# Kernel optimization log

Measured on AMD Instinct MI355X. Metric: run time of the kernel, lower is better.

Reference implementation:

```python
import jax, jax.numpy as jnp
import numpy as np

N_NODES = 50000
N_EDGES = 500000
N_FEAT = 128
EMB_DIM = 1024
HIDDEN = 128
OUT_DIM = 10
VOCAB = 55049
N_GRAPHS = 64


def setup_inputs() -> dict:
    key = jax.random.key(0)
    ks = jax.random.split(key, 12)
    x = jax.random.normal(ks[0], (N_NODES, N_FEAT), dtype=jnp.float32)
    edge_weight = jax.random.uniform(ks[1], (N_EDGES,), dtype=jnp.float32)
    edge_index = jax.random.randint(ks[2], (2, N_EDGES), 0, N_NODES)
    batch = jnp.sort(jax.random.randint(ks[3], (N_NODES,), 0, N_GRAPHS))
    node_ids = jax.random.randint(ks[4], (N_NODES,), 0, VOCAB)
    emb_table = jax.random.normal(ks[5], (VOCAB, EMB_DIM), dtype=jnp.float32)
    d_in = N_FEAT + EMB_DIM
    W1 = jax.random.normal(ks[6], (d_in, HIDDEN), dtype=jnp.float32) / np.sqrt(d_in)
    b1 = jnp.zeros((HIDDEN,), dtype=jnp.float32)
    W2 = jax.random.normal(ks[7], (HIDDEN, HIDDEN), dtype=jnp.float32) / np.sqrt(HIDDEN)
    b2 = jnp.zeros((HIDDEN,), dtype=jnp.float32)
    fcW = jax.random.normal(ks[8], (HIDDEN, OUT_DIM), dtype=jnp.float32) / np.sqrt(HIDDEN)
    fcb = jnp.zeros((OUT_DIM,), dtype=jnp.float32)
    return dict(x=x, edge_weight=edge_weight, emb_table=emb_table, W1=W1, b1=b1,
                W2=W2, b2=b2, fcW=fcW, fcb=fcb,
                edge_index=edge_index, batch=batch, node_ids=node_ids)


def gcn_conv(x, edge_index, edge_weight, W, b, n_nodes):
    # PyG GCNConv: x' = D^{-1/2} (A + I) D^{-1/2} (x W) + b, self-loop weight = 1
    x = x @ W
    src, dst = edge_index[0], edge_index[1]
    loop = jnp.arange(n_nodes)
    src = jnp.concatenate([src, loop])
    dst = jnp.concatenate([dst, loop])
    ew = jnp.concatenate([edge_weight, jnp.ones((n_nodes,), x.dtype)])
    deg = jax.ops.segment_sum(ew, dst, num_segments=n_nodes)
    dinv = jnp.where(deg > 0, jax.lax.rsqrt(deg), 0.0)
    norm = dinv[src] * ew * dinv[dst]  # [E+N]
    msgs = norm[:, None] * x[src]      # [E+N, H] gather
    out = jax.ops.segment_sum(msgs, dst, num_segments=n_nodes)  # scatter-add
    return out + b


def reference(x, edge_weight, emb_table, W1, b1, W2, b2, fcW, fcb,
              edge_index, batch, node_ids):
    n = x.shape[0]
    h = jnp.concatenate([x, emb_table[node_ids]], axis=1)  # [N, F+E]
    h = jax.nn.relu(gcn_conv(h, edge_index, edge_weight, W1, b1, n))
    h = jax.nn.relu(gcn_conv(h, edge_index, edge_weight, W2, b2, n))
    # global mean pool per graph (dropout is identity in eval)
    sums = jax.ops.segment_sum(h, batch, num_segments=N_GRAPHS)
    counts = jax.ops.segment_sum(jnp.ones((n,), h.dtype), batch, num_segments=N_GRAPHS)
    pooled = sums / jnp.maximum(counts, 1.0)[:, None]
    return pooled @ fcW + fcb
```

## Files before the change

kernel.cpp:

```cpp
#include <hip/hip_runtime.h>
#include <hip/hip_bf16.h>

#define N_NODES 50000
#define N_EDGES 500000
#define N_FEAT 128
#define EMB_DIM 1024
#define HIDDEN 128
#define OUT_DIM 10
#define N_GRAPHS 64
#define NB_NODE 196

typedef __attribute__((ext_vector_type(8))) short short8;
typedef __attribute__((ext_vector_type(4))) float f32x4;

__device__ __forceinline__ unsigned short f2bf(float f) {
    unsigned int u = __float_as_uint(f);
    return (unsigned short)((u + 0x7fffu + ((u >> 16) & 1u)) >> 16);
}
__device__ __forceinline__ float bflo(unsigned int r) { return __uint_as_float(r << 16); }
__device__ __forceinline__ float bfhi(unsigned int r) { return __uint_as_float(r & 0xffff0000u); }

__global__ __launch_bounds__(256) void k_init(float* __restrict__ deg,
                                              int* __restrict__ cnt,
                                              float* __restrict__ sums,
                                              float* __restrict__ counts) {
    int i = blockIdx.x * 256 + threadIdx.x;
    if (i < N_NODES) { deg[i] = 1.0f; cnt[i] = 0; }
    if (i < N_GRAPHS * HIDDEN) sums[i] = 0.0f;
    if (i < N_GRAPHS) counts[i] = 0.0f;
}

__global__ __launch_bounds__(256) void k_deg(const int* __restrict__ dst,
                                             const float* __restrict__ ew,
                                             float* __restrict__ deg,
                                             int* __restrict__ cnt) {
    int e = blockIdx.x * 256 + threadIdx.x;
    if (e < N_EDGES) {
        int d = dst[e];
        atomicAdd(&deg[d], ew[e]);
        atomicAdd(&cnt[d], 1);
    }
}

__global__ __launch_bounds__(256) void k_scan1(const int* __restrict__ cnt,
                                               int* __restrict__ bsum) {
    __shared__ int wsum[4];
    int i = blockIdx.x * 256 + threadIdx.x;
    int v = (i < N_NODES) ? cnt[i] : 0;
#pragma unroll
    for (int off = 32; off; off >>= 1) v += __shfl_down(v, off, 64);
    if ((threadIdx.x & 63) == 0) wsum[threadIdx.x >> 6] = v;
    __syncthreads();
    if (threadIdx.x == 0) bsum[blockIdx.x] = wsum[0] + wsum[1] + wsum[2] + wsum[3];
}

__global__ __launch_bounds__(256) void k_scan2(int* __restrict__ bsum) {
    __shared__ int sh[256];
    int t = threadIdx.x;
    int v = (t < NB_NODE) ? bsum[t] : 0;
    sh[t] = v;
    __syncthreads();
    for (int off = 1; off < 256; off <<= 1) {
        int add = (t >= off) ? sh[t - off] : 0;
        __syncthreads();
        sh[t] += add;
        __syncthreads();
    }
    if (t < NB_NODE) bsum[t] = sh[t] - v;
}

__global__ __launch_bounds__(256) void k_scan3(int* __restrict__ cntcur,
                                               const int* __restrict__ bofs,
                                               int* __restrict__ rowptr,
                                               float* __restrict__ dinv) {
    __shared__ int sh[256];
    const int t = threadIdx.x;
    const int i = blockIdx.x * 256 + t;
    int v = (i < N_NODES) ? cntcur[i] : 0;
    sh[t] = v;
    __syncthreads();
    for (int off = 1; off < 256; off <<= 1) {
        int add = (t >= off) ? sh[t - off] : 0;
        __syncthreads();
        sh[t] += add;
        __syncthreads();
    }
    int ex = sh[t] - v + bofs[blockIdx.x];
    if (i < N_NODES) {
        rowptr[i] = ex;
        cntcur[i] = ex;
        dinv[i] = 1.0f / sqrtf(dinv[i]);
    }
    if (i == 0) rowptr[N_NODES] = N_EDGES;
}

__global__ __launch_bounds__(256) void k_fill(const int* __restrict__ src,
                                              const int* __restrict__ dst,
                                              const float* __restrict__ ew,
                                              const float* __restrict__ dinv,
                                              int* __restrict__ cursor,
                                              int2* __restrict__ csr) {
    int e = blockIdx.x * 256 + threadIdx.x;
    if (e >= N_EDGES) return;
    int s = src[e], d = dst[e];
    int pos = atomicAdd(&cursor[d], 1);
    float norm = dinv[s] * ew[e] * dinv[d];
    csr[pos] = make_int2(s, __float_as_int(norm));
}

__device__ __forceinline__ void prep_one(const float* __restrict__ W,
                                         unsigned short* __restrict__ Wt,
                                         int K, int t) {
    int n = t & 127;
    int c = t >> 7;
    if (c * 16 >= K) return;
    short8 h0, h1;
#pragma unroll
    for (int i = 0; i < 16; i++) {
        unsigned short h = f2bf(W[(size_t)(c * 16 + i) * HIDDEN + n]);
        if (i < 8) h0[i] = (short)h;
        else       h1[i - 8] = (short)h;
    }
    size_t o = (size_t)n * K + c * 16;
    *(short8*)&Wt[o] = h0;
    *(short8*)&Wt[o + 8] = h1;
}

__global__ __launch_bounds__(256) void k_prep(const float* __restrict__ W1,
                                              unsigned short* __restrict__ Wt1,
                                              const float* __restrict__ W2,
                                              unsigned short* __restrict__ Wt2) {
    int b = blockIdx.x;
    if (b < 36) prep_one(W1, Wt1, N_FEAT + EMB_DIM, b * 256 + threadIdx.x);
    else        prep_one(W2, Wt2, HIDDEN, (b - 36) * 256 + threadIdx.x);
}

template <int MODE>
__global__ __launch_bounds__(256) void k_gemm(const float* __restrict__ X,
                                              const float* __restrict__ EMB,
                                              const int* __restrict__ ids,
                                              const unsigned short* __restrict__ Wt,
                                              unsigned short* __restrict__ tbf, int K) {
    __shared__ unsigned short As[128][40];
    __shared__ unsigned short Bs[128][40];

    const int tid = threadIdx.x;
    const int lane = tid & 63;
    const int wv = tid >> 6;
    const int wm = wv >> 1, wn = wv & 1;
    const int fr = lane & 15;
    const int fq = lane >> 4;
    const int mBase = blockIdx.x * 128;

    const int aRow = tid >> 1;
    const int aOff = (tid & 1) * 16;
    const int m = mBase + aRow;
    const int mc = (m < N_NODES) ? m : (N_NODES - 1);
    int embRow = 0;
    if (MODE == 0) embRow = ids[mc];

    f32x4 acc[4][4];
#pragma unroll
    for (int i = 0; i < 4; i++)
#pragma unroll
        for (int j = 0; j < 4; j++) acc[i][j] = (f32x4){0.f, 0.f, 0.f, 0.f};

    float av[16];
    short8 bh0, bh1;
    {
        const float* aptr = (MODE == 0)
            ? X + (size_t)mc * N_FEAT + aOff
            : X + (size_t)mc * HIDDEN + aOff;
        *(float4*)&av[0]  = *(const float4*)(aptr);
        *(float4*)&av[4]  = *(const float4*)(aptr + 4);
        *(float4*)&av[8]  = *(const float4*)(aptr + 8);
        *(float4*)&av[12] = *(const float4*)(aptr + 12);
        size_t bo = (size_t)aRow * K + aOff;
        bh0 = *(const short8*)&Wt[bo];
        bh1 = *(const short8*)&Wt[bo + 8];
    }

    for (int k0 = 0; k0 < K; k0 += 32) {
        short8 ah0, ah1;
#pragma unroll
        for (int i = 0; i < 16; i++) {
            float v = av[i];
            if (MODE == 1) v = fmaxf(v, 0.f);
            unsigned short h = f2bf(v);
            if (i < 8) ah0[i] = (short)h;
            else       ah1[i - 8] = (short)h;
        }
        *(short8*)&As[aRow][aOff] = ah0; *(short8*)&As[aRow][aOff + 8] = ah1;
        *(short8*)&Bs[aRow][aOff] = bh0; *(short8*)&Bs[aRow][aOff + 8] = bh1;
        __syncthreads();

        int k1 = k0 + 32;
        if (k1 < K) {
            const float* aptr;
            if (MODE == 0)
                aptr = (k1 < N_FEAT) ? X + (size_t)mc * N_FEAT + k1 + aOff
                                     : EMB + (size_t)embRow * EMB_DIM + (k1 - N_FEAT) + aOff;
            else
                aptr = X + (size_t)mc * HIDDEN + k1 + aOff;
            *(float4*)&av[0]  = *(const float4*)(aptr);
            *(float4*)&av[4]  = *(const float4*)(aptr + 4);
            *(float4*)&av[8]  = *(const float4*)(aptr + 8);
            *(float4*)&av[12] = *(const float4*)(aptr + 12);
            size_t bo = (size_t)aRow * K + k1 + aOff;
            bh0 = *(const short8*)&Wt[bo];
            bh1 = *(const short8*)&Wt[bo + 8];
        }

        short8 aF[4], bF[4];
#pragma unroll
        for (int i = 0; i < 4; i++) {
            aF[i] = *(const short8*)&As[wm * 64 + i * 16 + fr][fq * 8];
            bF[i] = *(const short8*)&Bs[wn * 64 + i * 16 + fr][fq * 8];
        }

#pragma unroll
        for (int i = 0; i < 4; i++)
#pragma unroll
            for (int j = 0; j < 4; j++)
                acc[i][j] = __builtin_amdgcn_mfma_f32_16x16x32_bf16(aF[i], bF[j], acc[i][j], 0, 0, 0);
        __syncthreads();
    }

#pragma unroll
    for (int i = 0; i < 4; i++) {
#pragma unroll
        for (int j = 0; j < 4; j++) {
            int gcol = wn * 64 + j * 16 + fr;
#pragma unroll
            for (int r = 0; r < 4; r++) {
                int grow = mBase + wm * 64 + i * 16 + fq * 4 + r;
                if (grow < N_NODES) tbf[(size_t)grow * HIDDEN + gcol] = f2bf(acc[i][j][r]);
            }
        }
    }
}

template <int POOL, int NWAVE>
__global__ __launch_bounds__(NWAVE * 64) void k_agg(const int2* __restrict__ csr,
                                                    const int* __restrict__ rowptr,
                                                    const float* __restrict__ dinv,
                                                    const unsigned short* __restrict__ tbf,
                                                    const float* __restrict__ bias,
                                                    const int* __restrict__ batch,
                                                    float* __restrict__ outp,
                                                    float* __restrict__ sums,
                                                    float* __restrict__ counts) {
    __shared__ float lsum[HIDDEN];
    __shared__ int lcnt;
    const int wv = threadIdx.x >> 6;
    const int lane = threadIdx.x & 63;
    const int n = blockIdx.x * NWAVE + wv;
    const unsigned int* t32 = (const unsigned int*)tbf;

    if (POOL) {
        if (threadIdx.x < HIDDEN) lsum[threadIdx.x] = 0.f;
        if (threadIdx.x == 0) lcnt = 0;
        __syncthreads();
    }

    float2 a = {0.f, 0.f};
    if (n < N_NODES) {
        const int beg = rowptr[n];
        const int end = rowptr[n + 1];
        const float di = dinv[n];
        const float sc = di * di;
        unsigned int sv = t32[(size_t)n * 64 + lane];
        float2 bv = ((const float2*)bias)[lane];
        a.x = fmaf(sc, bflo(sv), bv.x);
        a.y = fmaf(sc, bfhi(sv), bv.y);

        for (int base = beg; base < end; base += 64) {
            int cnt = end - base; if (cnt > 64) cnt = 64;
            int2 ce = (lane < cnt) ? csr[base + lane] : make_int2(0, 0);
            int j = 0;
            for (; j + 4 <= cnt; j += 4) {
                int s0 = __shfl(ce.x, j),     s1 = __shfl(ce.x, j + 1);
                int s2 = __shfl(ce.x, j + 2), s3 = __shfl(ce.x, j + 3);
                float w0 = __int_as_float(__shfl(ce.y, j));
                float w1 = __int_as_float(__shfl(ce.y, j + 1));
                float w2 = __int_as_float(__shfl(ce.y, j + 2));
                float w3 = __int_as_float(__shfl(ce.y, j + 3));
                unsigned int r0 = t32[(size_t)s0 * 64 + lane];
                unsigned int r1 = t32[(size_t)s1 * 64 + lane];
                unsigned int r2 = t32[(size_t)s2 * 64 + lane];
                unsigned int r3 = t32[(size_t)s3 * 64 + lane];
                a.x = fmaf(w0, bflo(r0), a.x); a.y = fmaf(w0, bfhi(r0), a.y);
                a.x = fmaf(w1, bflo(r1), a.x); a.y = fmaf(w1, bfhi(r1), a.y);
                a.x = fmaf(w2, bflo(r2), a.x); a.y = fmaf(w2, bfhi(r2), a.y);
                a.x = fmaf(w3, bflo(r3), a.x); a.y = fmaf(w3, bfhi(r3), a.y);
            }
            for (; j < cnt; j++) {
                int s0 = __shfl(ce.x, j);
                float w0 = __int_as_float(__shfl(ce.y, j));
                unsigned int r0 = t32[(size_t)s0 * 64 + lane];
                a.x = fmaf(w0, bflo(r0), a.x); a.y = fmaf(w0, bfhi(r0), a.y);
            }
        }
    }

    if (!POOL) {
        if (n < N_NODES) ((float2*)(outp + (size_t)n * HIDDEN))[lane] = a;
    } else {
        if (n < N_NODES) {
            a.x = fmaxf(a.x, 0.f);
            a.y = fmaxf(a.y, 0.f);
            int g = batch[n];
            int g0 = batch[blockIdx.x * NWAVE];
            if (g == g0) {
                atomicAdd(&lsum[lane * 2], a.x);
                atomicAdd(&lsum[lane * 2 + 1], a.y);
                if (lane == 0) atomicAdd(&lcnt, 1);
            } else {
                atomicAdd(&sums[g * HIDDEN + lane * 2], a.x);
                atomicAdd(&sums[g * HIDDEN + lane * 2 + 1], a.y);
                if (lane == 0) atomicAdd(&counts[g], 1.0f);
            }
        }
        __syncthreads();
        int g0 = batch[blockIdx.x * NWAVE];
        if (threadIdx.x < HIDDEN) atomicAdd(&sums[g0 * HIDDEN + threadIdx.x], lsum[threadIdx.x]);
        if (threadIdx.x == 0) atomicAdd(&counts[g0], (float)lcnt);
    }
}

__global__ __launch_bounds__(64) void k_final(const float* __restrict__ sums,
                                              const float* __restrict__ counts,
                                              const float* __restrict__ fcW,
                                              const float* __restrict__ fcb,
                                              float* __restrict__ out) {
    int g = blockIdx.x;
    int o = threadIdx.x;
    if (o >= OUT_DIM) return;
    float inv = 1.0f / fmaxf(counts[g], 1.0f);
    float acc = 0.f;
    for (int f = 0; f < HIDDEN; f++)
        acc = fmaf(sums[g * HIDDEN + f], fcW[f * OUT_DIM + o], acc);
    out[g * OUT_DIM + o] = acc * inv + fcb[o];
}

extern "C" void kernel_launch(void* const* d_in, const int* in_sizes, int n_in,
                              void* d_out, int out_size, void* d_ws, size_t ws_size,
                              hipStream_t stream) {
    const float* x      = (const float*)d_in[0];
    const float* ew     = (const float*)d_in[1];
    const float* emb    = (const float*)d_in[2];
    const float* W1     = (const float*)d_in[3];
    const float* b1     = (const float*)d_in[4];
    const float* W2     = (const float*)d_in[5];
    const float* b2     = (const float*)d_in[6];
    const float* fcW    = (const float*)d_in[7];
    const float* fcb    = (const float*)d_in[8];
    const int* edge_idx = (const int*)d_in[9];
    const int* batch    = (const int*)d_in[10];
    const int* node_ids = (const int*)d_in[11];
    float* out = (float*)d_out;

    const int* src = edge_idx;
    const int* dst = edge_idx + N_EDGES;

    float* ws     = (float*)d_ws;
    float* dinv   = ws;
    int*   cntcur = (int*)(ws + 50048);
    int*   rowptr = (int*)(ws + 100096);
    int*   bsum   = (int*)(ws + 150152);
    int2*  csr    = (int2*)(ws + 150408);
    unsigned short* tbf = (unsigned short*)(ws + 1150408);
    float* out1   = ws + 4350408;
    float* sums   = out1 + 6400000;
    float* counts = sums + N_GRAPHS * HIDDEN;
    unsigned short* wt1 = (unsigned short*)(ws + 10758664);
    unsigned short* wt2 = (unsigned short*)(ws + 10832392);

    const int NB_EDGE = (N_EDGES + 255) / 256;
    const int NB_GEMM = (N_NODES + 127) / 128;
    const int K1 = N_FEAT + EMB_DIM;

    k_init <<<NB_NODE, 256, 0, stream>>>(dinv, cntcur, sums, counts);
    k_deg  <<<NB_EDGE, 256, 0, stream>>>(dst, ew, dinv, cntcur);
    k_scan1<<<NB_NODE, 256, 0, stream>>>(cntcur, bsum);
    k_scan2<<<1, 256, 0, stream>>>(bsum);
    k_scan3<<<NB_NODE, 256, 0, stream>>>(cntcur, bsum, rowptr, dinv);
    k_fill <<<NB_EDGE, 256, 0, stream>>>(src, dst, ew, dinv, cntcur, csr);
    k_prep <<<40, 256, 0, stream>>>(W1, wt1, W2, wt2);

    k_gemm<0><<<NB_GEMM, 256, 0, stream>>>(x, emb, node_ids, wt1, tbf, K1);
    k_agg<0, 4><<<(N_NODES + 3) / 4, 256, 0, stream>>>(csr, rowptr, dinv, tbf, b1,
                                                       batch, out1, sums, counts);

    k_gemm<1><<<NB_GEMM, 256, 0, stream>>>(out1, nullptr, nullptr, wt2, tbf, HIDDEN);
    k_agg<1, 16><<<(N_NODES + 15) / 16, 1024, 0, stream>>>(csr, rowptr, dinv, tbf, b2,
                                                           batch, nullptr, sums, counts);

    k_final<<<N_GRAPHS, 64, 0, stream>>>(sums, counts, fcW, fcb, out);
}
```

Baseline: 549.0 us.

## Pack degree atomics, write layer-1 output as bf16, widen aggregation gathers

Degree and edge count are merged into one 64-bit atomic, with the edge weight stored as a 24-bit fixed-point fraction, so each edge does one atomic instead of two. The first aggregation now applies ReLU and stores bf16 instead of fp32, so the second GEMM reads bf16 directly and the intermediate buffer's traffic is halved. The aggregation kernels now split each wave into four 16-lane groups that each fetch a whole 128-bit row for a different edge, then combine the groups with cross-lane shuffles. Risks are fixed-point truncation error in the degree and bf16 rounding of the layer-1 output.

```diff
diff --git a/kernel.cpp b/kernel.cpp
--- a/kernel.cpp
+++ b/kernel.cpp
@@ -19,34 +19,34 @@
 }
 __device__ __forceinline__ float bflo(unsigned int r) { return __uint_as_float(r << 16); }
 __device__ __forceinline__ float bfhi(unsigned int r) { return __uint_as_float(r & 0xffff0000u); }
-
-__global__ __launch_bounds__(256) void k_init(float* __restrict__ deg,
-                                              int* __restrict__ cnt,
+__device__ __forceinline__ unsigned int packbf(float lo, float hi) {
+    return ((unsigned int)f2bf(hi) << 16) | f2bf(lo);
+}
+
+__global__ __launch_bounds__(256) void k_init(unsigned long long* __restrict__ dc,
                                               float* __restrict__ sums,
                                               float* __restrict__ counts) {
     int i = blockIdx.x * 256 + threadIdx.x;
-    if (i < N_NODES) { deg[i] = 1.0f; cnt[i] = 0; }
+    if (i < N_NODES) dc[i] = 0ULL;
     if (i < N_GRAPHS * HIDDEN) sums[i] = 0.0f;
     if (i < N_GRAPHS) counts[i] = 0.0f;
 }
 
 __global__ __launch_bounds__(256) void k_deg(const int* __restrict__ dst,
                                              const float* __restrict__ ew,
-                                             float* __restrict__ deg,
-                                             int* __restrict__ cnt) {
+                                             unsigned long long* __restrict__ dc) {
     int e = blockIdx.x * 256 + threadIdx.x;
     if (e < N_EDGES) {
-        int d = dst[e];
-        atomicAdd(&deg[d], ew[e]);
-        atomicAdd(&cnt[d], 1);
-    }
-}
-
-__global__ __launch_bounds__(256) void k_scan1(const int* __restrict__ cnt,
+        unsigned int fx = (unsigned int)(ew[e] * 16777216.0f);
+        atomicAdd(&dc[dst[e]], (1ULL << 32) | (unsigned long long)fx);
+    }
+}
+
+__global__ __launch_bounds__(256) void k_scan1(const unsigned long long* __restrict__ dc,
                                                int* __restrict__ bsum) {
     __shared__ int wsum[4];
     int i = blockIdx.x * 256 + threadIdx.x;
-    int v = (i < N_NODES) ? cnt[i] : 0;
+    int v = (i < N_NODES) ? (int)((const uint2*)dc)[i].y : 0;
 #pragma unroll
     for (int off = 32; off; off >>= 1) v += __shfl_down(v, off, 64);
     if ((threadIdx.x & 63) == 0) wsum[threadIdx.x >> 6] = v;
@@ -69,14 +69,16 @@
     if (t < NB_NODE) bsum[t] = sh[t] - v;
 }
 
-__global__ __launch_bounds__(256) void k_scan3(int* __restrict__ cntcur,
+__global__ __launch_bounds__(256) void k_scan3(const unsigned long long* __restrict__ dc,
                                                const int* __restrict__ bofs,
+                                               int* __restrict__ cursor,
                                                int* __restrict__ rowptr,
                                                float* __restrict__ dinv) {
     __shared__ int sh[256];
     const int t = threadIdx.x;
     const int i = blockIdx.x * 256 + t;
-    int v = (i < N_NODES) ? cntcur[i] : 0;
+    uint2 d = (i < N_NODES) ? ((const uint2*)dc)[i] : make_uint2(0u, 0u);
+    int v = (int)d.y;
     sh[t] = v;
     __syncthreads();
     for (int off = 1; off < 256; off <<= 1) {
@@ -88,8 +90,9 @@
     int ex = sh[t] - v + bofs[blockIdx.x];
     if (i < N_NODES) {
         rowptr[i] = ex;
-        cntcur[i] = ex;
-        dinv[i] = 1.0f / sqrtf(dinv[i]);
+        cursor[i] = ex;
+        float deg = 1.0f + (float)d.x * (1.0f / 16777216.0f);
+        dinv[i] = 1.0f / sqrtf(deg);
     }
     if (i == 0) rowptr[N_NODES] = N_EDGES;
 }
@@ -137,6 +140,7 @@
 
 template <int MODE>
 __global__ __launch_bounds__(256) void k_gemm(const float* __restrict__ X,
+                                              const unsigned short* __restrict__ Xb,
                                               const float* __restrict__ EMB,
                                               const int* __restrict__ ids,
                                               const unsigned short* __restrict__ Wt,
@@ -166,46 +170,56 @@
         for (int j = 0; j < 4; j++) acc[i][j] = (f32x4){0.f, 0.f, 0.f, 0.f};
 
     float av[16];
+    short8 axb0, axb1;
     short8 bh0, bh1;
     {
-        const float* aptr = (MODE == 0)
-            ? X + (size_t)mc * N_FEAT + aOff
-            : X + (size_t)mc * HIDDEN + aOff;
-        *(float4*)&av[0]  = *(const float4*)(aptr);
-        *(float4*)&av[4]  = *(const float4*)(aptr + 4);
-        *(float4*)&av[8]  = *(const float4*)(aptr + 8);
-        *(float4*)&av[12] = *(const float4*)(aptr + 12);
-        size_t bo = (size_t)aRow * K + aOff;
-        bh0 = *(const short8*)&Wt[bo];
-        bh1 = *(const short8*)&Wt[bo + 8];
-    }
-
-    for (int k0 = 0; k0 < K; k0 += 32) {
-        short8 ah0, ah1;
-#pragma unroll
-        for (int i = 0; i < 16; i++) {
-            float v = av[i];
-            if (MODE == 1) v = fmaxf(v, 0.f);
-            unsigned short h = f2bf(v);
-            if (i < 8) ah0[i] = (short)h;
-            else       ah1[i - 8] = (short)h;
-        }
-        *(short8*)&As[aRow][aOff] = ah0; *(short8*)&As[aRow][aOff + 8] = ah1;
-        *(short8*)&Bs[aRow][aOff] = bh0; *(short8*)&Bs[aRow][aOff + 8] = bh1;
-        __syncthreads();
-
-        int k1 = k0 + 32;
-        if (k1 < K) {
-            const float* aptr;
-            if (MODE == 0)
-                aptr = (k1 < N_FEAT) ? X + (size_t)mc * N_FEAT + k1 + aOff
-                                     : EMB + (size_t)embRow * EMB_DIM + (k1 - N_FEAT) + aOff;
-            else
-                aptr = X + (size_t)mc * HIDDEN + k1 + aOff;
+        if (MODE == 0) {
+            const float* aptr = X + (size_t)mc * N_FEAT + aOff;
             *(float4*)&av[0]  = *(const float4*)(aptr);
             *(float4*)&av[4]  = *(const float4*)(aptr + 4);
             *(float4*)&av[8]  = *(const float4*)(aptr + 8);
             *(float4*)&av[12] = *(const float4*)(aptr + 12);
+        } else {
+            const unsigned short* aptr = Xb + (size_t)mc * HIDDEN + aOff;
+            axb0 = *(const short8*)(aptr);
+            axb1 = *(const short8*)(aptr + 8);
+        }
+        size_t bo = (size_t)aRow * K + aOff;
+        bh0 = *(const short8*)&Wt[bo];
+        bh1 = *(const short8*)&Wt[bo + 8];
+    }
+
+    for (int k0 = 0; k0 < K; k0 += 32) {
+        short8 ah0, ah1;
+        if (MODE == 0) {
+#pragma unroll
+            for (int i = 0; i < 16; i++) {
+                unsigned short h = f2bf(av[i]);
+                if (i < 8) ah0[i] = (short)h;
+                else       ah1[i - 8] = (short)h;
+            }
+        } else {
+            ah0 = axb0; ah1 = axb1;
+        }
+        *(short8*)&As[aRow][aOff] = ah0; *(short8*)&As[aRow][aOff + 8] = ah1;
+        *(short8*)&Bs[aRow][aOff] = bh0; *(short8*)&Bs[aRow][aOff + 8] = bh1;
+        __syncthreads();
+
+        int k1 = k0 + 32;
+        if (k1 < K) {
+            if (MODE == 0) {
+                const float* aptr = (k1 < N_FEAT)
+                    ? X + (size_t)mc * N_FEAT + k1 + aOff
+                    : EMB + (size_t)embRow * EMB_DIM + (k1 - N_FEAT) + aOff;
+                *(float4*)&av[0]  = *(const float4*)(aptr);
+                *(float4*)&av[4]  = *(const float4*)(aptr + 4);
+                *(float4*)&av[8]  = *(const float4*)(aptr + 8);
+                *(float4*)&av[12] = *(const float4*)(aptr + 12);
+            } else {
+                const unsigned short* aptr = Xb + (size_t)mc * HIDDEN + k1 + aOff;
+                axb0 = *(const short8*)(aptr);
+                axb1 = *(const short8*)(aptr + 8);
+            }
             size_t bo = (size_t)aRow * K + k1 + aOff;
             bh0 = *(const short8*)&Wt[bo];
             bh1 = *(const short8*)&Wt[bo + 8];
@@ -247,15 +261,17 @@
                                                     const unsigned short* __restrict__ tbf,
                                                     const float* __restrict__ bias,
                                                     const int* __restrict__ batch,
-                                                    float* __restrict__ outp,
+                                                    unsigned short* __restrict__ outb,
                                                     float* __restrict__ sums,
                                                     float* __restrict__ counts) {
     __shared__ float lsum[HIDDEN];
     __shared__ int lcnt;
     const int wv = threadIdx.x >> 6;
     const int lane = threadIdx.x & 63;
+    const int grp = lane >> 4;
+    const int q = lane & 15;
     const int n = blockIdx.x * NWAVE + wv;
-    const unsigned int* t32 = (const unsigned int*)tbf;
+    const uint4* t128 = (const uint4*)tbf;
 
     if (POOL) {
         if (threadIdx.x < HIDDEN) lsum[threadIdx.x] = 0.f;
@@ -263,61 +279,86 @@
         __syncthreads();
     }
 
-    float2 a = {0.f, 0.f};
+    float acc[8] = {};
     if (n < N_NODES) {
         const int beg = rowptr[n];
         const int end = rowptr[n + 1];
         const float di = dinv[n];
-        const float sc = di * di;
-        unsigned int sv = t32[(size_t)n * 64 + lane];
-        float2 bv = ((const float2*)bias)[lane];
-        a.x = fmaf(sc, bflo(sv), bv.x);
-        a.y = fmaf(sc, bfhi(sv), bv.y);
+        const float wself = (grp == 0) ? di * di : 0.f;
+        uint4 sr = t128[(size_t)n * 16 + q];
+        acc[0] = wself * bflo(sr.x); acc[1] = wself * bfhi(sr.x);
+        acc[2] = wself * bflo(sr.y); acc[3] = wself * bfhi(sr.y);
+        acc[4] = wself * bflo(sr.z); acc[5] = wself * bfhi(sr.z);
+        acc[6] = wself * bflo(sr.w); acc[7] = wself * bfhi(sr.w);
+        if (grp == 0) {
+            float4 b0 = ((const float4*)bias)[q * 2];
+            float4 b1 = ((const float4*)bias)[q * 2 + 1];
+            acc[0] += b0.x; acc[1] += b0.y; acc[2] += b0.z; acc[3] += b0.w;
+            acc[4] += b1.x; acc[5] += b1.y; acc[6] += b1.z; acc[7] += b1.w;
+        }
 
         for (int base = beg; base < end; base += 64) {
             int cnt = end - base; if (cnt > 64) cnt = 64;
             int2 ce = (lane < cnt) ? csr[base + lane] : make_int2(0, 0);
             int j = 0;
-            for (; j + 4 <= cnt; j += 4) {
-                int s0 = __shfl(ce.x, j),     s1 = __shfl(ce.x, j + 1);
-                int s2 = __shfl(ce.x, j + 2), s3 = __shfl(ce.x, j + 3);
-                float w0 = __int_as_float(__shfl(ce.y, j));
-                float w1 = __int_as_float(__shfl(ce.y, j + 1));
-                float w2 = __int_as_float(__shfl(ce.y, j + 2));
-                float w3 = __int_as_float(__shfl(ce.y, j + 3));
-                unsigned int r0 = t32[(size_t)s0 * 64 + lane];
-                unsigned int r1 = t32[(size_t)s1 * 64 + lane];
-                unsigned int r2 = t32[(size_t)s2 * 64 + lane];
-                unsigned int r3 = t32[(size_t)s3 * 64 + lane];
-                a.x = fmaf(w0, bflo(r0), a.x); a.y = fmaf(w0, bfhi(r0), a.y);
-                a.x = fmaf(w1, bflo(r1), a.x); a.y = fmaf(w1, bfhi(r1), a.y);
-                a.x = fmaf(w2, bflo(r2), a.x); a.y = fmaf(w2, bfhi(r2), a.y);
-                a.x = fmaf(w3, bflo(r3), a.x); a.y = fmaf(w3, bfhi(r3), a.y);
-            }
-            for (; j < cnt; j++) {
-                int s0 = __shfl(ce.x, j);
-                float w0 = __int_as_float(__shfl(ce.y, j));
-                unsigned int r0 = t32[(size_t)s0 * 64 + lane];
-                a.x = fmaf(w0, bflo(r0), a.x); a.y = fmaf(w0, bfhi(r0), a.y);
-            }
-        }
+            for (; j + 8 <= cnt; j += 8) {
+                int   sA = __shfl(ce.x, j + grp);
+                float wA = __int_as_float(__shfl(ce.y, j + grp));
+                int   sB = __shfl(ce.x, j + 4 + grp);
+                float wB = __int_as_float(__shfl(ce.y, j + 4 + grp));
+                uint4 rA = t128[(size_t)sA * 16 + q];
+                uint4 rB = t128[(size_t)sB * 16 + q];
+                acc[0] = fmaf(wA, bflo(rA.x), acc[0]); acc[1] = fmaf(wA, bfhi(rA.x), acc[1]);
+                acc[2] = fmaf(wA, bflo(rA.y), acc[2]); acc[3] = fmaf(wA, bfhi(rA.y), acc[3]);
+                acc[4] = fmaf(wA, bflo(rA.z), acc[4]); acc[5] = fmaf(wA, bfhi(rA.z), acc[5]);
+                acc[6] = fmaf(wA, bflo(rA.w), acc[6]); acc[7] = fmaf(wA, bfhi(rA.w), acc[7]);
+                acc[0] = fmaf(wB, bflo(rB.x), acc[0]); acc[1] = fmaf(wB, bfhi(rB.x), acc[1]);
+                acc[2] = fmaf(wB, bflo(rB.y), acc[2]); acc[3] = fmaf(wB, bfhi(rB.y), acc[3]);
+                acc[4] = fmaf(wB, bflo(rB.z), acc[4]); acc[5] = fmaf(wB, bfhi(rB.z), acc[5]);
+                acc[6] = fmaf(wB, bflo(rB.w), acc[6]); acc[7] = fmaf(wB, bfhi(rB.w), acc[7]);
+            }
+            for (; j < cnt; j += 4) {
+                int   s = __shfl(ce.x, j + grp);
+                float w = __int_as_float(__shfl(ce.y, j + grp));
+                uint4 r = t128[(size_t)s * 16 + q];
+                acc[0] = fmaf(w, bflo(r.x), acc[0]); acc[1] = fmaf(w, bfhi(r.x), acc[1]);
+                acc[2] = fmaf(w, bflo(r.y), acc[2]); acc[3] = fmaf(w, bfhi(r.y), acc[3]);
+                acc[4] = fmaf(w, bflo(r.z), acc[4]); acc[5] = fmaf(w, bfhi(r.z), acc[5]);
+                acc[6] = fmaf(w, bflo(r.w), acc[6]); acc[7] = fmaf(w, bfhi(r.w), acc[7]);
+            }
+        }
+    }
+
+#pragma unroll
+    for (int i = 0; i < 8; i++) {
+        acc[i] += __shfl_xor(acc[i], 16);
+        acc[i] += __shfl_xor(acc[i], 32);
     }
 
     if (!POOL) {
-        if (n < N_NODES) ((float2*)(outp + (size_t)n * HIDDEN))[lane] = a;
+        if (n < N_NODES && grp == 0) {
+#pragma unroll
+            for (int i = 0; i < 8; i++) acc[i] = fmaxf(acc[i], 0.f);
+            uint4 o;
+            o.x = packbf(acc[0], acc[1]);
+            o.y = packbf(acc[2], acc[3]);
+            o.z = packbf(acc[4], acc[5]);
+            o.w = packbf(acc[6], acc[7]);
+            ((uint4*)outb)[(size_t)n * 16 + q] = o;
+        }
     } else {
-        if (n < N_NODES) {
-            a.x = fmaxf(a.x, 0.f);
-            a.y = fmaxf(a.y, 0.f);
+        if (n < N_NODES && grp == 0) {
+#pragma unroll
+            for (int i = 0; i < 8; i++) acc[i] = fmaxf(acc[i], 0.f);
             int g = batch[n];
             int g0 = batch[blockIdx.x * NWAVE];
             if (g == g0) {
-                atomicAdd(&lsum[lane * 2], a.x);
-                atomicAdd(&lsum[lane * 2 + 1], a.y);
+#pragma unroll
+                for (int i = 0; i < 8; i++) atomicAdd(&lsum[q * 8 + i], acc[i]);
                 if (lane == 0) atomicAdd(&lcnt, 1);
             } else {
-                atomicAdd(&sums[g * HIDDEN + lane * 2], a.x);
-                atomicAdd(&sums[g * HIDDEN + lane * 2 + 1], a.y);
+#pragma unroll
+                for (int i = 0; i < 8; i++) atomicAdd(&sums[g * HIDDEN + q * 8 + i], acc[i]);
                 if (lane == 0) atomicAdd(&counts[g], 1.0f);
             }
         }
@@ -365,34 +406,35 @@
 
     float* ws     = (float*)d_ws;
     float* dinv   = ws;
-    int*   cntcur = (int*)(ws + 50048);
-    int*   rowptr = (int*)(ws + 100096);
-    int*   bsum   = (int*)(ws + 150152);
-    int2*  csr    = (int2*)(ws + 150408);
-    unsigned short* tbf = (unsigned short*)(ws + 1150408);
-    float* out1   = ws + 4350408;
-    float* sums   = out1 + 6400000;
+    unsigned long long* dc = (unsigned long long*)(ws + 50048);
+    int*   cursor = (int*)(ws + 150048);
+    int*   rowptr = (int*)(ws + 200096);
+    int*   bsum   = (int*)(ws + 250152);
+    int2*  csr    = (int2*)(ws + 250408);
+    unsigned short* tbf   = (unsigned short*)(ws + 1250408);
+    unsigned short* out1b = (unsigned short*)(ws + 4450408);
+    float* sums   = ws + 7650408;
     float* counts = sums + N_GRAPHS * HIDDEN;
-    unsigned short* wt1 = (unsigned short*)(ws + 10758664);
-    unsigned short* wt2 = (unsigned short*)(ws + 10832392);
+    unsigned short* wt1 = (unsigned short*)(ws + 7658664);
+    unsigned short* wt2 = (unsigned short*)(ws + 7732392);
 
     const int NB_EDGE = (N_EDGES + 255) / 256;
     const int NB_GEMM = (N_NODES + 127) / 128;
     const int K1 = N_FEAT + EMB_DIM;
 
-    k_init <<<NB_NODE, 256, 0, stream>>>(dinv, cntcur, sums, counts);
-    k_deg  <<<NB_EDGE, 256, 0, stream>>>(dst, ew, dinv, cntcur);
-    k_scan1<<<NB_NODE, 256, 0, stream>>>(cntcur, bsum);
+    k_init <<<NB_NODE, 256, 0, stream>>>(dc, sums, counts);
+    k_deg  <<<NB_EDGE, 256, 0, stream>>>(dst, ew, dc);
+    k_scan1<<<NB_NODE, 256, 0, stream>>>(dc, bsum);
     k_scan2<<<1, 256, 0, stream>>>(bsum);
-    k_scan3<<<NB_NODE, 256, 0, stream>>>(cntcur, bsum, rowptr, dinv);
-    k_fill <<<NB_EDGE, 256, 0, stream>>>(src, dst, ew, dinv, cntcur, csr);
+    k_scan3<<<NB_NODE, 256, 0, stream>>>(dc, bsum, cursor, rowptr, dinv);
+    k_fill <<<NB_EDGE, 256, 0, stream>>>(src, dst, ew, dinv, cursor, csr);
     k_prep <<<40, 256, 0, stream>>>(W1, wt1, W2, wt2);
 
-    k_gemm<0><<<NB_GEMM, 256, 0, stream>>>(x, emb, node_ids, wt1, tbf, K1);
+    k_gemm<0><<<NB_GEMM, 256, 0, stream>>>(x, nullptr, emb, node_ids, wt1, tbf, K1);
     k_agg<0, 4><<<(N_NODES + 3) / 4, 256, 0, stream>>>(csr, rowptr, dinv, tbf, b1,
-                                                       batch, out1, sums, counts);
-
-    k_gemm<1><<<NB_GEMM, 256, 0, stream>>>(out1, nullptr, nullptr, wt2, tbf, HIDDEN);
+                                                       batch, out1b, sums, counts);
+
+    k_gemm<1><<<NB_GEMM, 256, 0, stream>>>(nullptr, out1b, nullptr, nullptr, wt2, tbf, HIDDEN);
     k_agg<1, 16><<<(N_NODES + 15) / 16, 1024, 0, stream>>>(csr, rowptr, dinv, tbf, b2,
                                                            batch, nullptr, sums, counts);
 
```

After: 522.8 us. 1.05x faster.
